# Kernel tuning notes

Measured on AMD Instinct MI355X. Metric: run time of the kernel, lower is better.

## Reference

```python
import jax, jax.numpy as jnp
import numpy as np

N = 100000
E = 3200000
OC = 16


def _lin_params(key, out_c, in_c, bias=True):
    k1, k2 = jax.random.split(key)
    s = 1.0 / np.sqrt(in_c)
    w = jax.random.uniform(k1, (out_c, in_c), jnp.float32, -s, s)
    b = jax.random.uniform(k2, (out_c,), jnp.float32, -s, s) if bias else None
    return w, b


def setup_inputs() -> dict:
    key = jax.random.key(0)
    ks = jax.random.split(key, 16)
    o = jax.random.normal(ks[0], (N, 2), jnp.float32)
    m = jax.random.normal(ks[1], (N, 2), jnp.float32)
    c = jax.random.uniform(ks[2], (N, 2), jnp.float32)
    ei_o = jax.random.randint(ks[3], (2, E), 0, N, jnp.int32)
    ei_m = jax.random.randint(ks[4], (2, E), 0, N, jnp.int32)
    ei_c = jax.random.randint(ks[5], (2, E), 0, N, jnp.int32)
    w1r, b1 = _lin_params(ks[6], 8, 2)
    w1s, _ = _lin_params(ks[7], 8, 2, bias=False)
    w2r, b2 = _lin_params(ks[8], OC, 8)
    w2s, _ = _lin_params(ks[9], OC, 8, bias=False)
    w3r, b3 = _lin_params(ks[10], OC, 2)
    w3s, _ = _lin_params(ks[11], OC, 2, bias=False)
    w4r, b4 = _lin_params(ks[12], 2, OC * 3)
    w4s, _ = _lin_params(ks[13], 2, OC * 3, bias=False)
    return dict(o=o, m=m, c=c, edge_index_o=ei_o, edge_index_m=ei_m, edge_index_c=ei_c,
                w1r=w1r, w1s=w1s, b1=b1, w2r=w2r, w2s=w2s, b2=b2,
                w3r=w3r, w3s=w3s, b3=b3, w4r=w4r, w4s=w4s, b4=b4)


def graph_conv(x, edge_index, w_rel, w_root, b):
    # PyG GraphConv, aggr='add': out_i = W_rel * sum_{j->i} x_j + b + W_root * x_i
    src, dst = edge_index[0], edge_index[1]
    agg = jax.ops.segment_sum(x[src], dst, num_segments=x.shape[0])
    return agg @ w_rel.T + b + x @ w_root.T


def forward_prior(x, ei, w1r, w1s, b1, w2r, w2s, b2):
    # dropout is identity in eval mode
    x = jax.nn.elu(graph_conv(x, ei, w1r, w1s, b1))
    return graph_conv(x, ei, w2r, w2s, b2)


def reference(o, m, c, edge_index_o, edge_index_m, edge_index_c,
              w1r, w1s, b1, w2r, w2s, b2, w3r, w3s, b3, w4r, w4s, b4):
    o_out = forward_prior(o, edge_index_o, w1r, w1s, b1, w2r, w2s, b2)
    o_feat = jnp.max(o_out, axis=0, keepdims=True)  # global_max_pool, single graph
    m_out = forward_prior(m, edge_index_m, w1r, w1s, b1, w2r, w2s, b2)
    m_feat = jnp.max(m_out, axis=0, keepdims=True)
    prior = jnp.concatenate([o_feat, m_feat], axis=1)  # [1, 2*OC]
    x = jax.nn.elu(graph_conv(c, edge_index_c, w3r, w3s, b3))  # [N, OC]
    x = jnp.concatenate([x, jnp.broadcast_to(prior, (c.shape[0], prior.shape[1]))], axis=1)
    x = graph_conv(x, edge_index_c, w4r, w4s, b4)
    return jax.nn.sigmoid(x) + c
```

## Files before the change

kernel.cpp:

```cpp
#include <hip/hip_runtime.h>
#include <float.h>
#include <math.h>


#define BBITS   8
#define BINSZ   256
#define MAXP    512
#define SRCBITS 17
#define SRCMASK ((1 << SRCBITS) - 1)
#define CAP     9216
#define EPT     8
#define EPT2    9

__device__ __forceinline__ float eluf(float x) {
  return x > 0.0f ? x : (expf(x) - 1.0f);
}

__device__ __forceinline__ void atomicMaxF(float* addr, float val) {
  int* ia = (int*)addr;
  int old = *ia;
  while (__int_as_float(old) < val) {
    int assumed = old;
    old = atomicCAS(ia, assumed, __float_as_int(val));
    if (old == assumed) break;
  }
}


__device__ __forceinline__ void place_body(const int* __restrict__ ei, int e, int P,
                                           int* __restrict__ binCnt, int* __restrict__ buf,
                                           int blk) {
  __shared__ int h[MAXP];
  __shared__ int base[MAXP];
  int t = threadIdx.x;
  for (int i = t; i < P; i += 1024) h[i] = 0;
  __syncthreads();
  const int* src = ei;
  const int* dst = ei + e;
  int lo = blk * (1024 * EPT);
  int v[EPT], bb[EPT], r[EPT];
#pragma unroll
  for (int k = 0; k < EPT; k++) {
    int idx = lo + k * 1024 + t;
    bool ok = idx < e;
    int d = ok ? dst[idx] : 0;
    int s = ok ? src[idx] : 0;
    bb[k] = ok ? (d >> BBITS) : -1;
    v[k] = ((d & (BINSZ - 1)) << SRCBITS) | s;
    r[k] = (bb[k] >= 0) ? atomicAdd(&h[bb[k]], 1) : 0;
  }
  __syncthreads();
  for (int i = t; i < P; i += 1024)
    base[i] = h[i] ? atomicAdd(&binCnt[i], h[i]) : 0;
  __syncthreads();
#pragma unroll
  for (int k = 0; k < EPT; k++) {
    if (bb[k] >= 0) {
      int idx = base[bb[k]] + r[k];
      if (idx < CAP) buf[(size_t)bb[k] * CAP + idx] = v[k];
    }
  }
}

__device__ __forceinline__ void sort_body(const int* __restrict__ binCnt,
                                          int* __restrict__ buf,
                                          int* __restrict__ rowBeg, int* __restrict__ rowEnd,
                                          int n, int p) {
  __shared__ int cnt[BINSZ];
  __shared__ int sc[BINSZ];
  int t = threadIdx.x;
  int nEd = min(binCnt[p], CAP);
  int* pk = buf + (size_t)p * CAP;
  if (t < BINSZ) cnt[t] = 0;
  __syncthreads();
  int v[EPT2], r[EPT2];
#pragma unroll
  for (int k = 0; k < EPT2; k++) {
    int i = k * 1024 + t;
    bool ok = i < nEd;
    v[k] = ok ? pk[i] : 0;
    r[k] = ok ? atomicAdd(&cnt[v[k] >> SRCBITS], 1) : -1;
  }
  __syncthreads();
  if (t < BINSZ) sc[t] = cnt[t];
  __syncthreads();
  for (int d = 1; d < BINSZ; d <<= 1) {
    int x = 0;
    if (t < BINSZ && t >= d) x = sc[t - d];
    __syncthreads();
    if (t < BINSZ) sc[t] += x;
    __syncthreads();
  }
  if (t < BINSZ) {
    int node = p * BINSZ + t;
    if (node < n) {
      int beg = p * CAP + sc[t] - cnt[t];
      rowBeg[node] = beg;
      rowEnd[node] = beg + cnt[t];
    }
  }
  __syncthreads();
#pragma unroll
  for (int k = 0; k < EPT2; k++) {
    if (r[k] >= 0) {
      int loc = v[k] >> SRCBITS;
      pk[sc[loc] - cnt[loc] + r[k]] = v[k] & SRCMASK;
    }
  }
}

__device__ __forceinline__ void agg1om_body(const int* __restrict__ rowBeg,
                                            const int* __restrict__ rowEnd,
                                            const int* __restrict__ src,
                                            const float* __restrict__ x,
                                            const float* __restrict__ wr,
                                            const float* __restrict__ b,
                                            const float* __restrict__ wo,
                                            float* __restrict__ xh8, int n, int tid) {
  int i = tid >> 3, j = tid & 7;
  if (i >= n) return;
  int r0 = rowBeg[i], r1 = rowEnd[i];
  float ax = 0.f, ay = 0.f;
  for (int e2 = r0 + j; e2 < r1; e2 += 8) {
    int s = src[e2];
    float2 v = ((const float2*)x)[s];
    ax += v.x;
    ay += v.y;
  }
  ax += __shfl_xor(ax, 1); ax += __shfl_xor(ax, 2); ax += __shfl_xor(ax, 4);
  ay += __shfl_xor(ay, 1); ay += __shfl_xor(ay, 2); ay += __shfl_xor(ay, 4);
  float2 xv = ((const float2*)x)[i];
  float v = eluf(wr[2 * j] * ax + wr[2 * j + 1] * ay + b[j] + wo[2 * j] * xv.x + wo[2 * j + 1] * xv.y);
  xh8[(size_t)i * 8 + j] = v;
}

__device__ __forceinline__ void agg2pool_body(const int* __restrict__ rowBeg,
                                              const int* __restrict__ rowEnd,
                                              const int* __restrict__ src,
                                              const float* __restrict__ x8,
                                              const float* __restrict__ wr,
                                              const float* __restrict__ b,
                                              const float* __restrict__ wo,
                                              float* __restrict__ bmax, int n,
                                              int tid, int aggblk) {
  __shared__ float wmax[16][16];
  int i = tid >> 3, j = tid & 7;
  float a[8] = {0, 0, 0, 0, 0, 0, 0, 0};
  bool valid = (i < n);
  if (valid) {
    int r0 = rowBeg[i], r1 = rowEnd[i];
    for (int e2 = r0 + j; e2 < r1; e2 += 8) {
      int s = src[e2];
      const float4* xp = (const float4*)(x8 + (size_t)s * 8);
      float4 v0 = xp[0], v1 = xp[1];
      a[0] += v0.x; a[1] += v0.y; a[2] += v0.z; a[3] += v0.w;
      a[4] += v1.x; a[5] += v1.y; a[6] += v1.z; a[7] += v1.w;
    }
  }
#pragma unroll
  for (int k = 0; k < 8; k++) {
    a[k] += __shfl_xor(a[k], 1);
    a[k] += __shfl_xor(a[k], 2);
    a[k] += __shfl_xor(a[k], 4);
  }
  float o0, o1;
  if (valid) {
    const float4* xp = (const float4*)(x8 + (size_t)i * 8);
    float4 x0 = xp[0], x1 = xp[1];
    float xx[8] = {x0.x, x0.y, x0.z, x0.w, x1.x, x1.y, x1.z, x1.w};
    int k0 = 2 * j, k1 = 2 * j + 1;
    o0 = b[k0];
    o1 = b[k1];
#pragma unroll
    for (int l = 0; l < 8; l++) {
      o0 += wr[8 * k0 + l] * a[l] + wo[8 * k0 + l] * xx[l];
      o1 += wr[8 * k1 + l] * a[l] + wo[8 * k1 + l] * xx[l];
    }
  } else {
    o0 = o1 = -FLT_MAX;
  }
#pragma unroll
  for (int d = 8; d < 64; d <<= 1) {
    o0 = fmaxf(o0, __shfl_xor(o0, d));
    o1 = fmaxf(o1, __shfl_xor(o1, d));
  }
  int wid = threadIdx.x >> 6, lane = threadIdx.x & 63;
  if (lane < 8) {
    wmax[wid][2 * lane] = o0;
    wmax[wid][2 * lane + 1] = o1;
  }
  __syncthreads();
  if (threadIdx.x < 16) {
    float v = -FLT_MAX;
#pragma unroll
    for (int w = 0; w < 16; w++) v = fmaxf(v, wmax[w][threadIdx.x]);
    bmax[(size_t)aggblk * 16 + threadIdx.x] = v;
  }
}


__global__ __launch_bounds__(1024) void place_k(const int* __restrict__ ei, int e, int P,
                                                int* __restrict__ binCnt, int* __restrict__ buf) {
  place_body(ei, e, P, binCnt, buf, blockIdx.x);
}

__global__ __launch_bounds__(1024) void sort_k(const int* __restrict__ binCnt,
                                               int* __restrict__ buf,
                                               int* __restrict__ rowBeg, int* __restrict__ rowEnd,
                                               int n) {
  sort_body(binCnt, buf, rowBeg, rowEnd, n, blockIdx.x);
}

__global__ __launch_bounds__(1024) void place_agg1_k(const int* __restrict__ eiX, int e, int P,
                                                     int* __restrict__ binCntX, int* __restrict__ bufX,
                                                     int EBP,
                                                     const int* __restrict__ rowBegY,
                                                     const int* __restrict__ rowEndY,
                                                     const int* __restrict__ srcY,
                                                     const float* __restrict__ xY,
                                                     const float* __restrict__ wr,
                                                     const float* __restrict__ b,
                                                     const float* __restrict__ wo,
                                                     float* __restrict__ xh8Y, int n) {
  if ((int)blockIdx.x < EBP) {
    place_body(eiX, e, P, binCntX, bufX, blockIdx.x);
    return;
  }
  int tid = (blockIdx.x - EBP) * 1024 + threadIdx.x;
  agg1om_body(rowBegY, rowEndY, srcY, xY, wr, b, wo, xh8Y, n, tid);
}

__global__ __launch_bounds__(1024) void sort_agg2_k(const int* __restrict__ binCntX,
                                                    int* __restrict__ bufX,
                                                    int* __restrict__ rowBegX,
                                                    int* __restrict__ rowEndX,
                                                    int n, int P,
                                                    const int* __restrict__ rowBegY,
                                                    const int* __restrict__ rowEndY,
                                                    const int* __restrict__ srcY,
                                                    const float* __restrict__ x8Y,
                                                    const float* __restrict__ wr,
                                                    const float* __restrict__ b,
                                                    const float* __restrict__ wo,
                                                    float* __restrict__ bmaxY) {
  if ((int)blockIdx.x < P) {
    sort_body(binCntX, bufX, rowBegX, rowEndX, n, blockIdx.x);
    return;
  }
  int aggblk = blockIdx.x - P;
  int tid = aggblk * 1024 + threadIdx.x;
  agg2pool_body(rowBegY, rowEndY, srcY, x8Y, wr, b, wo, bmaxY, n, tid, aggblk);
}

__global__ __launch_bounds__(1024) void agg1c_reduce_k(const float* __restrict__ bmax,
                                                       float* __restrict__ feats, int nb,
                                                       const int* __restrict__ rowBeg,
                                                       const int* __restrict__ rowEnd,
                                                       const int* __restrict__ src,
                                                       const float* __restrict__ cin,
                                                       const float* __restrict__ wr,
                                                       const float* __restrict__ b,
                                                       const float* __restrict__ wo,
                                                       const float* __restrict__ w4r,
                                                       const float* __restrict__ w4s,
                                                       float* __restrict__ yrel,
                                                       float* __restrict__ yroot, int n) {
  if (blockIdx.x == 0) {
    __shared__ float red[512];
    int t = threadIdx.x;
    if (t < 512) {
      int ch = t & 31, row = t >> 5;
      int g = ch >> 4, k = ch & 15;
      float v = -FLT_MAX;
      for (int blk = row; blk < nb; blk += 16)
        v = fmaxf(v, bmax[((size_t)g * nb + blk) * 16 + k]);
      red[t] = v;
    }
    __syncthreads();
    if (t < 32) {
      float m = red[t];
#pragma unroll
      for (int r = 1; r < 16; r++) m = fmaxf(m, red[t + 32 * r]);
      feats[t] = m;
    }
    return;
  }
  int tid = (blockIdx.x - 1) * 1024 + threadIdx.x;
  int i = tid >> 3, j = tid & 7;
  if (i >= n) return;
  int r0 = rowBeg[i], r1 = rowEnd[i];
  float ax = 0.f, ay = 0.f;
  for (int e2 = r0 + j; e2 < r1; e2 += 8) {
    int s = src[e2];
    float2 v = ((const float2*)cin)[s];
    ax += v.x;
    ay += v.y;
  }
  ax += __shfl_xor(ax, 1); ax += __shfl_xor(ax, 2); ax += __shfl_xor(ax, 4);
  ay += __shfl_xor(ay, 1); ay += __shfl_xor(ay, 2); ay += __shfl_xor(ay, 4);
  float2 xv = ((const float2*)cin)[i];
  float yr0 = 0.f, yr1 = 0.f, ys0 = 0.f, ys1 = 0.f;
#pragma unroll
  for (int kk = 0; kk < 2; kk++) {
    int k = 2 * j + kk;
    float v = eluf(wr[2 * k] * ax + wr[2 * k + 1] * ay + b[k] + wo[2 * k] * xv.x + wo[2 * k + 1] * xv.y);
    yr0 += w4r[k] * v;
    yr1 += w4r[48 + k] * v;
    ys0 += w4s[k] * v;
    ys1 += w4s[48 + k] * v;
  }
  yr0 += __shfl_xor(yr0, 1); yr0 += __shfl_xor(yr0, 2); yr0 += __shfl_xor(yr0, 4);
  yr1 += __shfl_xor(yr1, 1); yr1 += __shfl_xor(yr1, 2); yr1 += __shfl_xor(yr1, 4);
  ys0 += __shfl_xor(ys0, 1); ys0 += __shfl_xor(ys0, 2); ys0 += __shfl_xor(ys0, 4);
  ys1 += __shfl_xor(ys1, 1); ys1 += __shfl_xor(ys1, 2); ys1 += __shfl_xor(ys1, 4);
  if (j == 0) ((float2*)yrel)[i] = make_float2(yr0, yr1);
  if (j == 1) ((float2*)yroot)[i] = make_float2(ys0, ys1);
}

__global__ __launch_bounds__(1024) void aggfinal_k(const int* __restrict__ rowBeg,
                                                   const int* __restrict__ rowEnd,
                                                   const int* __restrict__ src,
                                                   const float* __restrict__ yrel,
                                                   const float* __restrict__ yroot,
                                                   const float* __restrict__ cin,
                                                   const float* __restrict__ feats,
                                                   const float* __restrict__ w4r,
                                                   const float* __restrict__ b4,
                                                   const float* __restrict__ w4s,
                                                   float* __restrict__ out, int n) {
  int tid = blockIdx.x * 1024 + threadIdx.x;
  int i = tid >> 3, j = tid & 7;
  if (i >= n) return;
  int r0 = rowBeg[i], r1 = rowEnd[i];
  float ay0 = 0.f, ay1 = 0.f;
  for (int e2 = r0 + j; e2 < r1; e2 += 8) {
    int s = src[e2];
    float2 v = ((const float2*)yrel)[s];
    ay0 += v.x;
    ay1 += v.y;
  }
  ay0 += __shfl_xor(ay0, 1); ay0 += __shfl_xor(ay0, 2); ay0 += __shfl_xor(ay0, 4);
  ay1 += __shfl_xor(ay1, 1); ay1 += __shfl_xor(ay1, 2); ay1 += __shfl_xor(ay1, 4);
  if (j != 0) return;
  float pr0 = 0.f, pr1 = 0.f, ps0 = 0.f, ps1 = 0.f;
#pragma unroll
  for (int k = 0; k < 32; k++) {
    float pv = feats[k];
    pr0 += w4r[16 + k] * pv;
    pr1 += w4r[64 + k] * pv;
    ps0 += w4s[16 + k] * pv;
    ps1 += w4s[64 + k] * pv;
  }
  float d = (float)(r1 - r0);
  float2 yrt = ((const float2*)yroot)[i];
  float acc0 = b4[0] + ps0 + d * pr0 + ay0 + yrt.x;
  float acc1 = b4[1] + ps1 + d * pr1 + ay1 + yrt.y;
  float2 cv = ((const float2*)cin)[i];
  float o0 = 1.0f / (1.0f + expf(-acc0)) + cv.x;
  float o1 = 1.0f / (1.0f + expf(-acc1)) + cv.y;
  ((float2*)out)[i] = make_float2(o0, o1);
}


__global__ void init_feats_k(float* feats) {
  int t = threadIdx.x;
  if (t < 32) feats[t] = -FLT_MAX;
}

__global__ void scatter2_k(const float* __restrict__ x, const int* __restrict__ ei,
                           float* __restrict__ agg, float* __restrict__ deg, int e) {
  int idx = blockIdx.x * blockDim.x + threadIdx.x;
  if (idx >= e) return;
  int s = ei[idx];
  int d = ei[e + idx];
  float2 v = ((const float2*)x)[s];
  atomicAdd(&agg[2 * d + 0], v.x);
  atomicAdd(&agg[2 * d + 1], v.y);
  if (deg) atomicAdd(&deg[d], 1.0f);
}

__global__ void scatter8_k(const float* __restrict__ x, const int* __restrict__ ei,
                           float* __restrict__ agg, int e) {
  int idx = blockIdx.x * blockDim.x + threadIdx.x;
  if (idx >= e) return;
  int s = ei[idx];
  int d = ei[e + idx];
  const float4* xp = (const float4*)(x + (size_t)s * 8);
  float4 v0 = xp[0], v1 = xp[1];
  float* ap = agg + (size_t)d * 8;
  atomicAdd(ap + 0, v0.x); atomicAdd(ap + 1, v0.y);
  atomicAdd(ap + 2, v0.z); atomicAdd(ap + 3, v0.w);
  atomicAdd(ap + 4, v1.x); atomicAdd(ap + 5, v1.y);
  atomicAdd(ap + 6, v1.z); atomicAdd(ap + 7, v1.w);
}

__global__ void scatter16_k(const float* __restrict__ x, const int* __restrict__ ei,
                            float* __restrict__ agg, int e) {
  int idx = blockIdx.x * blockDim.x + threadIdx.x;
  if (idx >= e) return;
  int s = ei[idx];
  int d = ei[e + idx];
  const float4* xp = (const float4*)(x + (size_t)s * 16);
  float4 v0 = xp[0], v1 = xp[1], v2 = xp[2], v3 = xp[3];
  float* ap = agg + (size_t)d * 16;
  atomicAdd(ap + 0,  v0.x); atomicAdd(ap + 1,  v0.y);
  atomicAdd(ap + 2,  v0.z); atomicAdd(ap + 3,  v0.w);
  atomicAdd(ap + 4,  v1.x); atomicAdd(ap + 5,  v1.y);
  atomicAdd(ap + 6,  v1.z); atomicAdd(ap + 7,  v1.w);
  atomicAdd(ap + 8,  v2.x); atomicAdd(ap + 9,  v2.y);
  atomicAdd(ap + 10, v2.z); atomicAdd(ap + 11, v2.w);
  atomicAdd(ap + 12, v3.x); atomicAdd(ap + 13, v3.y);
  atomicAdd(ap + 14, v3.z); atomicAdd(ap + 15, v3.w);
}

__global__ void node_2to8_elu_k(const float* __restrict__ agg, const float* __restrict__ xin,
                                const float* __restrict__ wr, const float* __restrict__ b,
                                const float* __restrict__ wo, float* __restrict__ xout, int n) {
  int i = blockIdx.x * blockDim.x + threadIdx.x;
  if (i >= n) return;
  float2 a = ((const float2*)agg)[i];
  float2 x = ((const float2*)xin)[i];
  float out[8];
#pragma unroll
  for (int k = 0; k < 8; k++)
    out[k] = eluf(wr[2 * k] * a.x + wr[2 * k + 1] * a.y + b[k] + wo[2 * k] * x.x + wo[2 * k + 1] * x.y);
  float4* op = (float4*)(xout + (size_t)i * 8);
  op[0] = make_float4(out[0], out[1], out[2], out[3]);
  op[1] = make_float4(out[4], out[5], out[6], out[7]);
}

__global__ void node_2to16_elu_k(const float* __restrict__ agg, const float* __restrict__ xin,
                                 const float* __restrict__ wr, const float* __restrict__ b,
                                 const float* __restrict__ wo, float* __restrict__ xout, int n) {
  int i = blockIdx.x * blockDim.x + threadIdx.x;
  if (i >= n) return;
  float2 a = ((const float2*)agg)[i];
  float2 x = ((const float2*)xin)[i];
  float out[16];
#pragma unroll
  for (int k = 0; k < 16; k++)
    out[k] = eluf(wr[2 * k] * a.x + wr[2 * k + 1] * a.y + b[k] + wo[2 * k] * x.x + wo[2 * k + 1] * x.y);
  float4* op = (float4*)(xout + (size_t)i * 16);
  op[0] = make_float4(out[0],  out[1],  out[2],  out[3]);
  op[1] = make_float4(out[4],  out[5],  out[6],  out[7]);
  op[2] = make_float4(out[8],  out[9],  out[10], out[11]);
  op[3] = make_float4(out[12], out[13], out[14], out[15]);
}

__global__ void conv2_pool_atomic_k(const float* __restrict__ agg, const float* __restrict__ x8,
                                    const float* __restrict__ wr, const float* __restrict__ b,
                                    const float* __restrict__ wo, float* __restrict__ feat, int n) {
  int i = blockIdx.x * blockDim.x + threadIdx.x;
  float out[16];
  if (i < n) {
    const float4* ap = (const float4*)(agg + (size_t)i * 8);
    const float4* xp = (const float4*)(x8 + (size_t)i * 8);
    float4 a0 = ap[0], a1 = ap[1];
    float4 x0 = xp[0], x1 = xp[1];
    float a[8] = {a0.x, a0.y, a0.z, a0.w, a1.x, a1.y, a1.z, a1.w};
    float x[8] = {x0.x, x0.y, x0.z, x0.w, x1.x, x1.y, x1.z, x1.w};
#pragma unroll
    for (int k = 0; k < 16; k++) {
      float v = b[k];
#pragma unroll
      for (int j = 0; j < 8; j++) v += wr[8 * k + j] * a[j] + wo[8 * k + j] * x[j];
      out[k] = v;
    }
  } else {
#pragma unroll
    for (int k = 0; k < 16; k++) out[k] = -FLT_MAX;
  }
#pragma unroll
  for (int k = 0; k < 16; k++) {
    float v = out[k];
    for (int off = 32; off >= 1; off >>= 1) v = fmaxf(v, __shfl_xor(v, off));
    if ((threadIdx.x & 63) == 0) atomicMaxF(&feat[k], v);
  }
}

__global__ void final_atomic_k(const float* __restrict__ agg16, const float* __restrict__ x16,
                               const float* __restrict__ deg, const float* __restrict__ cin,
                               const float* __restrict__ feats, const float* __restrict__ w4r,
                               const float* __restrict__ b4, const float* __restrict__ w4s,
                               float* __restrict__ out, int n) {
  int i = blockIdx.x * blockDim.x + threadIdx.x;
  if (i >= n) return;
  float pr0 = 0.f, pr1 = 0.f, ps0 = 0.f, ps1 = 0.f;
#pragma unroll
  for (int k = 0; k < 32; k++) {
    float pv = feats[k];
    pr0 += w4r[16 + k] * pv;
    pr1 += w4r[48 + 16 + k] * pv;
    ps0 += w4s[16 + k] * pv;
    ps1 += w4s[48 + 16 + k] * pv;
  }
  float d = deg[i];
  float acc0 = b4[0] + ps0 + d * pr0;
  float acc1 = b4[1] + ps1 + d * pr1;
  const float* ag = agg16 + (size_t)i * 16;
  const float* xv = x16 + (size_t)i * 16;
#pragma unroll
  for (int k = 0; k < 16; k++) {
    float a = ag[k], x = xv[k];
    acc0 += w4r[k] * a + w4s[k] * x;
    acc1 += w4r[48 + k] * a + w4s[48 + k] * x;
  }
  float2 cv = ((const float2*)cin)[i];
  float o0 = 1.0f / (1.0f + expf(-acc0)) + cv.x;
  float o1 = 1.0f / (1.0f + expf(-acc1)) + cv.y;
  ((float2*)out)[i] = make_float2(o0, o1);
}


extern "C" void kernel_launch(void* const* d_in, const int* in_sizes, int n_in,
                              void* d_out, int out_size, void* d_ws, size_t ws_size,
                              hipStream_t stream) {
  const float* o   = (const float*)d_in[0];
  const float* m   = (const float*)d_in[1];
  const float* c   = (const float*)d_in[2];
  const int* ei_o  = (const int*)d_in[3];
  const int* ei_m  = (const int*)d_in[4];
  const int* ei_c  = (const int*)d_in[5];
  const float* w1r = (const float*)d_in[6];
  const float* w1s = (const float*)d_in[7];
  const float* b1  = (const float*)d_in[8];
  const float* w2r = (const float*)d_in[9];
  const float* w2s = (const float*)d_in[10];
  const float* b2  = (const float*)d_in[11];
  const float* w3r = (const float*)d_in[12];
  const float* w3s = (const float*)d_in[13];
  const float* b3  = (const float*)d_in[14];
  const float* w4r = (const float*)d_in[15];
  const float* w4s = (const float*)d_in[16];
  const float* b4  = (const float*)d_in[17];

  const int n = in_sizes[0] / 2;
  const int e = in_sizes[3] / 2;
  const int P = (n + BINSZ - 1) >> BBITS;

  const int EBP = (e + 1024 * EPT - 1) / (1024 * EPT);
  const int G1  = (8 * n + 1023) / 1024;

  size_t off = 0;
  int* bufA = (int*)d_ws;                           off += (size_t)P * CAP * 4;
  int* bufB = (int*)((char*)d_ws + off);            off += (size_t)P * CAP * 4;
  int* rowBegA = (int*)((char*)d_ws + off);         off += (size_t)n * 4;
  int* rowEndA = (int*)((char*)d_ws + off);         off += (size_t)n * 4;
  int* rowBegB = (int*)((char*)d_ws + off);         off += (size_t)n * 4;
  int* rowEndB = (int*)((char*)d_ws + off);         off += (size_t)n * 4;
  float* xh8o = (float*)((char*)d_ws + off);        off += (size_t)n * 8 * 4;
  float* xh8m = (float*)((char*)d_ws + off);        off += (size_t)n * 8 * 4;
  float* bmax = (float*)((char*)d_ws + off);        off += (size_t)2 * G1 * 16 * 4;
  int* binCnt3 = (int*)((char*)d_ws + off);         off += (size_t)3 * MAXP * 4;
  float* feats = (float*)((char*)d_ws + off);       off += 32 * 4;

  float* yrel  = xh8o;
  float* yroot = xh8o + (size_t)2 * n;

  bool csr_ok = (off <= ws_size) && (P <= MAXP) && (n <= (1 << SRCBITS));

  if (!csr_ok) {
    const int BS = 256;
    const int nbn = (n + BS - 1) / BS;
    float* agg_f   = (float*)d_ws;
    float* xh_f    = agg_f + (size_t)n * 16;
    float* deg_f   = xh_f + (size_t)n * 16;
    float* feats_f = deg_f + n;
    const int nb_e = (e + BS - 1) / BS;
    init_feats_k<<<1, 64, 0, stream>>>(feats_f);
    hipMemsetAsync(agg_f, 0, (size_t)n * 2 * sizeof(float), stream);
    scatter2_k<<<nb_e, BS, 0, stream>>>(o, ei_o, agg_f, nullptr, e);
    node_2to8_elu_k<<<nbn, BS, 0, stream>>>(agg_f, o, w1r, b1, w1s, xh_f, n);
    hipMemsetAsync(agg_f, 0, (size_t)n * 8 * sizeof(float), stream);
    scatter8_k<<<nb_e, BS, 0, stream>>>(xh_f, ei_o, agg_f, e);
    conv2_pool_atomic_k<<<nbn, BS, 0, stream>>>(agg_f, xh_f, w2r, b2, w2s, feats_f, n);
    hipMemsetAsync(agg_f, 0, (size_t)n * 2 * sizeof(float), stream);
    scatter2_k<<<nb_e, BS, 0, stream>>>(m, ei_m, agg_f, nullptr, e);
    node_2to8_elu_k<<<nbn, BS, 0, stream>>>(agg_f, m, w1r, b1, w1s, xh_f, n);
    hipMemsetAsync(agg_f, 0, (size_t)n * 8 * sizeof(float), stream);
    scatter8_k<<<nb_e, BS, 0, stream>>>(xh_f, ei_m, agg_f, e);
    conv2_pool_atomic_k<<<nbn, BS, 0, stream>>>(agg_f, xh_f, w2r, b2, w2s, feats_f + 16, n);
    hipMemsetAsync(agg_f, 0, (size_t)n * 2 * sizeof(float), stream);
    hipMemsetAsync(deg_f, 0, (size_t)n * sizeof(float), stream);
    scatter2_k<<<nb_e, BS, 0, stream>>>(c, ei_c, agg_f, deg_f, e);
    node_2to16_elu_k<<<nbn, BS, 0, stream>>>(agg_f, c, w3r, b3, w3s, xh_f, n);
    hipMemsetAsync(agg_f, 0, (size_t)n * 16 * sizeof(float), stream);
    scatter16_k<<<nb_e, BS, 0, stream>>>(xh_f, ei_c, agg_f, e);
    final_atomic_k<<<nbn, BS, 0, stream>>>(agg_f, xh_f, deg_f, c, feats_f, w4r, b4, w4s,
                                           (float*)d_out, n);
    return;
  }

  int* bcO = binCnt3;
  int* bcM = binCnt3 + MAXP;
  int* bcC = binCnt3 + 2 * MAXP;

  hipMemsetAsync(binCnt3, 0, (size_t)3 * MAXP * sizeof(int), stream);

  place_k<<<EBP, 1024, 0, stream>>>(ei_o, e, P, bcO, bufA);
  sort_k<<<P, 1024, 0, stream>>>(bcO, bufA, rowBegA, rowEndA, n);

  place_agg1_k<<<EBP + G1, 1024, 0, stream>>>(ei_m, e, P, bcM, bufB, EBP,
                                              rowBegA, rowEndA, bufA, o,
                                              w1r, b1, w1s, xh8o, n);
  sort_agg2_k<<<P + G1, 1024, 0, stream>>>(bcM, bufB, rowBegB, rowEndB, n, P,
                                           rowBegA, rowEndA, bufA, xh8o,
                                           w2r, b2, w2s, bmax);

  place_agg1_k<<<EBP + G1, 1024, 0, stream>>>(ei_c, e, P, bcC, bufA, EBP,
                                              rowBegB, rowEndB, bufB, m,
                                              w1r, b1, w1s, xh8m, n);
  sort_agg2_k<<<P + G1, 1024, 0, stream>>>(bcC, bufA, rowBegA, rowEndA, n, P,
                                           rowBegB, rowEndB, bufB, xh8m,
                                           w2r, b2, w2s, bmax + (size_t)G1 * 16);

  agg1c_reduce_k<<<1 + G1, 1024, 0, stream>>>(bmax, feats, G1,
                                              rowBegA, rowEndA, bufA, c,
                                              w3r, b3, w3s, w4r, w4s,
                                              yrel, yroot, n);
  aggfinal_k<<<G1, 1024, 0, stream>>>(rowBegA, rowEndA, bufA, yrel, yroot, c,
                                      feats, w4r, b4, w4s, (float*)d_out, n);
}
```

Before: 279.1 us.

## Add third CSR buffer to deepen cross-graph pipeline of sort/place/aggregate kernels

Allocates a third bucket buffer so the CSR build for graph c no longer has to wait for graph o's buffer to be freed. The independent stages of the three graphs (place, sort, agg1, agg2, agg1c) are then packed into fewer, wider fused launches: 7 kernels instead of 8, with more concurrent blocks each. The global feature reduction is split into its own small kernel. This costs more workspace, and a fallback two-buffer schedule is kept for when the workspace is too small.

```diff
diff --git a/kernel.cpp b/kernel.cpp
--- a/kernel.cpp
+++ b/kernel.cpp
@@ -198,94 +198,17 @@
   }
 }
 
-
-__global__ __launch_bounds__(1024) void place_k(const int* __restrict__ ei, int e, int P,
-                                                int* __restrict__ binCnt, int* __restrict__ buf) {
-  place_body(ei, e, P, binCnt, buf, blockIdx.x);
-}
-
-__global__ __launch_bounds__(1024) void sort_k(const int* __restrict__ binCnt,
-                                               int* __restrict__ buf,
-                                               int* __restrict__ rowBeg, int* __restrict__ rowEnd,
-                                               int n) {
-  sort_body(binCnt, buf, rowBeg, rowEnd, n, blockIdx.x);
-}
-
-__global__ __launch_bounds__(1024) void place_agg1_k(const int* __restrict__ eiX, int e, int P,
-                                                     int* __restrict__ binCntX, int* __restrict__ bufX,
-                                                     int EBP,
-                                                     const int* __restrict__ rowBegY,
-                                                     const int* __restrict__ rowEndY,
-                                                     const int* __restrict__ srcY,
-                                                     const float* __restrict__ xY,
-                                                     const float* __restrict__ wr,
-                                                     const float* __restrict__ b,
-                                                     const float* __restrict__ wo,
-                                                     float* __restrict__ xh8Y, int n) {
-  if ((int)blockIdx.x < EBP) {
-    place_body(eiX, e, P, binCntX, bufX, blockIdx.x);
-    return;
-  }
-  int tid = (blockIdx.x - EBP) * 1024 + threadIdx.x;
-  agg1om_body(rowBegY, rowEndY, srcY, xY, wr, b, wo, xh8Y, n, tid);
-}
-
-__global__ __launch_bounds__(1024) void sort_agg2_k(const int* __restrict__ binCntX,
-                                                    int* __restrict__ bufX,
-                                                    int* __restrict__ rowBegX,
-                                                    int* __restrict__ rowEndX,
-                                                    int n, int P,
-                                                    const int* __restrict__ rowBegY,
-                                                    const int* __restrict__ rowEndY,
-                                                    const int* __restrict__ srcY,
-                                                    const float* __restrict__ x8Y,
-                                                    const float* __restrict__ wr,
-                                                    const float* __restrict__ b,
-                                                    const float* __restrict__ wo,
-                                                    float* __restrict__ bmaxY) {
-  if ((int)blockIdx.x < P) {
-    sort_body(binCntX, bufX, rowBegX, rowEndX, n, blockIdx.x);
-    return;
-  }
-  int aggblk = blockIdx.x - P;
-  int tid = aggblk * 1024 + threadIdx.x;
-  agg2pool_body(rowBegY, rowEndY, srcY, x8Y, wr, b, wo, bmaxY, n, tid, aggblk);
-}
-
-__global__ __launch_bounds__(1024) void agg1c_reduce_k(const float* __restrict__ bmax,
-                                                       float* __restrict__ feats, int nb,
-                                                       const int* __restrict__ rowBeg,
-                                                       const int* __restrict__ rowEnd,
-                                                       const int* __restrict__ src,
-                                                       const float* __restrict__ cin,
-                                                       const float* __restrict__ wr,
-                                                       const float* __restrict__ b,
-                                                       const float* __restrict__ wo,
-                                                       const float* __restrict__ w4r,
-                                                       const float* __restrict__ w4s,
-                                                       float* __restrict__ yrel,
-                                                       float* __restrict__ yroot, int n) {
-  if (blockIdx.x == 0) {
-    __shared__ float red[512];
-    int t = threadIdx.x;
-    if (t < 512) {
-      int ch = t & 31, row = t >> 5;
-      int g = ch >> 4, k = ch & 15;
-      float v = -FLT_MAX;
-      for (int blk = row; blk < nb; blk += 16)
-        v = fmaxf(v, bmax[((size_t)g * nb + blk) * 16 + k]);
-      red[t] = v;
-    }
-    __syncthreads();
-    if (t < 32) {
-      float m = red[t];
-#pragma unroll
-      for (int r = 1; r < 16; r++) m = fmaxf(m, red[t + 32 * r]);
-      feats[t] = m;
-    }
-    return;
-  }
-  int tid = (blockIdx.x - 1) * 1024 + threadIdx.x;
+__device__ __forceinline__ void agg1c_body(const int* __restrict__ rowBeg,
+                                           const int* __restrict__ rowEnd,
+                                           const int* __restrict__ src,
+                                           const float* __restrict__ cin,
+                                           const float* __restrict__ wr,
+                                           const float* __restrict__ b,
+                                           const float* __restrict__ wo,
+                                           const float* __restrict__ w4r,
+                                           const float* __restrict__ w4s,
+                                           float* __restrict__ yrel,
+                                           float* __restrict__ yroot, int n, int tid) {
   int i = tid >> 3, j = tid & 7;
   if (i >= n) return;
   int r0 = rowBeg[i], r1 = rowEnd[i];
@@ -315,6 +238,103 @@
   ys1 += __shfl_xor(ys1, 1); ys1 += __shfl_xor(ys1, 2); ys1 += __shfl_xor(ys1, 4);
   if (j == 0) ((float2*)yrel)[i] = make_float2(yr0, yr1);
   if (j == 1) ((float2*)yroot)[i] = make_float2(ys0, ys1);
+}
+
+
+__global__ __launch_bounds__(1024) void place_k(const int* __restrict__ ei, int e, int P,
+                                                int* __restrict__ binCnt, int* __restrict__ buf) {
+  place_body(ei, e, P, binCnt, buf, blockIdx.x);
+}
+
+__global__ __launch_bounds__(1024) void k_sort_place(const int* __restrict__ bcX,
+                                                     int* __restrict__ bufX,
+                                                     int* __restrict__ rbX, int* __restrict__ reX,
+                                                     int n, int P,
+                                                     const int* __restrict__ eiY, int e,
+                                                     int* __restrict__ bcY, int* __restrict__ bufY) {
+  int b = blockIdx.x;
+  if (b < P) { sort_body(bcX, bufX, rbX, reX, n, b); return; }
+  place_body(eiY, e, P, bcY, bufY, b - P);
+}
+
+__global__ __launch_bounds__(1024) void k_sort_place_agg1(
+    int nS, int nPl,
+    const int* __restrict__ bcY, int* __restrict__ bufY,
+    int* __restrict__ rbY, int* __restrict__ reY, int n, int P,
+    const int* __restrict__ eiZ, int e,
+    int* __restrict__ bcZ, int* __restrict__ bufZ,
+    const int* __restrict__ rbX, const int* __restrict__ reX,
+    const int* __restrict__ srcX, const float* __restrict__ xX,
+    const float* __restrict__ w1r, const float* __restrict__ b1,
+    const float* __restrict__ w1s, float* __restrict__ xh8X) {
+  int b = blockIdx.x;
+  if (b < nS) { sort_body(bcY, bufY, rbY, reY, n, b); return; }
+  b -= nS;
+  if (b < nPl) { place_body(eiZ, e, P, bcZ, bufZ, b); return; }
+  b -= nPl;
+  agg1om_body(rbX, reX, srcX, xX, w1r, b1, w1s, xh8X, n, b * 1024 + threadIdx.x);
+}
+
+__global__ __launch_bounds__(1024) void k_sort_agg1_agg2(
+    int nS, int nA1,
+    const int* __restrict__ bcZ, int* __restrict__ bufZ,
+    int* __restrict__ rbZ, int* __restrict__ reZ, int n, int P,
+    const int* __restrict__ rbY, const int* __restrict__ reY,
+    const int* __restrict__ srcY, const float* __restrict__ xY,
+    const float* __restrict__ w1r, const float* __restrict__ b1,
+    const float* __restrict__ w1s, float* __restrict__ xh8Y,
+    const int* __restrict__ rbX, const int* __restrict__ reX,
+    const int* __restrict__ srcX, const float* __restrict__ x8X,
+    const float* __restrict__ w2r, const float* __restrict__ b2,
+    const float* __restrict__ w2s, float* __restrict__ bmaxX) {
+  int b = blockIdx.x;
+  if (b < nS) { sort_body(bcZ, bufZ, rbZ, reZ, n, b); return; }
+  b -= nS;
+  if (b < nA1) { agg1om_body(rbY, reY, srcY, xY, w1r, b1, w1s, xh8Y, n, b * 1024 + threadIdx.x); return; }
+  b -= nA1;
+  agg2pool_body(rbX, reX, srcX, x8X, w2r, b2, w2s, bmaxX, n, b * 1024 + threadIdx.x, b);
+}
+
+__global__ __launch_bounds__(1024) void k_agg1c_agg2(
+    int nA1c,
+    const int* __restrict__ rbC, const int* __restrict__ reC,
+    const int* __restrict__ srcC, const float* __restrict__ cin,
+    const float* __restrict__ w3r, const float* __restrict__ b3,
+    const float* __restrict__ w3s,
+    const float* __restrict__ w4r, const float* __restrict__ w4s,
+    float* __restrict__ yrel, float* __restrict__ yroot, int n,
+    const int* __restrict__ rbY, const int* __restrict__ reY,
+    const int* __restrict__ srcY, const float* __restrict__ x8Y,
+    const float* __restrict__ w2r, const float* __restrict__ b2,
+    const float* __restrict__ w2s, float* __restrict__ bmaxY) {
+  int b = blockIdx.x;
+  if (b < nA1c) {
+    agg1c_body(rbC, reC, srcC, cin, w3r, b3, w3s, w4r, w4s, yrel, yroot, n,
+               b * 1024 + threadIdx.x);
+    return;
+  }
+  b -= nA1c;
+  agg2pool_body(rbY, reY, srcY, x8Y, w2r, b2, w2s, bmaxY, n,
+                b * 1024 + threadIdx.x, b);
+}
+
+__global__ void reduce_feats_k(const float* __restrict__ bmax, float* __restrict__ feats,
+                               int nb) {
+  __shared__ float red[512];
+  int t = threadIdx.x;
+  int ch = t & 31, row = t >> 5;
+  int g = ch >> 4, k = ch & 15;
+  float v = -FLT_MAX;
+  for (int blk = row; blk < nb; blk += 16)
+    v = fmaxf(v, bmax[((size_t)g * nb + blk) * 16 + k]);
+  red[t] = v;
+  __syncthreads();
+  if (t < 32) {
+    float m = red[t];
+#pragma unroll
+    for (int r = 1; r < 16; r++) m = fmaxf(m, red[t + 32 * r]);
+    feats[t] = m;
+  }
 }
 
 __global__ __launch_bounds__(1024) void aggfinal_k(const int* __restrict__ rowBeg,
@@ -541,25 +561,116 @@
   const int EBP = (e + 1024 * EPT - 1) / (1024 * EPT);
   const int G1  = (8 * n + 1023) / 1024;
 
-  size_t off = 0;
-  int* bufA = (int*)d_ws;                           off += (size_t)P * CAP * 4;
-  int* bufB = (int*)((char*)d_ws + off);            off += (size_t)P * CAP * 4;
-  int* rowBegA = (int*)((char*)d_ws + off);         off += (size_t)n * 4;
-  int* rowEndA = (int*)((char*)d_ws + off);         off += (size_t)n * 4;
-  int* rowBegB = (int*)((char*)d_ws + off);         off += (size_t)n * 4;
-  int* rowEndB = (int*)((char*)d_ws + off);         off += (size_t)n * 4;
-  float* xh8o = (float*)((char*)d_ws + off);        off += (size_t)n * 8 * 4;
-  float* xh8m = (float*)((char*)d_ws + off);        off += (size_t)n * 8 * 4;
-  float* bmax = (float*)((char*)d_ws + off);        off += (size_t)2 * G1 * 16 * 4;
-  int* binCnt3 = (int*)((char*)d_ws + off);         off += (size_t)3 * MAXP * 4;
-  float* feats = (float*)((char*)d_ws + off);       off += 32 * 4;
+  const size_t slab = (size_t)P * CAP * 4;
+
+  size_t off3 = 0;
+  int* bufA = (int*)d_ws;                            off3 += slab;
+  int* bufB = (int*)((char*)d_ws + off3);            off3 += slab;
+  int* bufC = (int*)((char*)d_ws + off3);            off3 += slab;
+  int* rbA = (int*)((char*)d_ws + off3);             off3 += (size_t)n * 4;
+  int* reA = (int*)((char*)d_ws + off3);             off3 += (size_t)n * 4;
+  int* rbB = (int*)((char*)d_ws + off3);             off3 += (size_t)n * 4;
+  int* reB = (int*)((char*)d_ws + off3);             off3 += (size_t)n * 4;
+  int* rbC = (int*)((char*)d_ws + off3);             off3 += (size_t)n * 4;
+  int* reC = (int*)((char*)d_ws + off3);             off3 += (size_t)n * 4;
+  float* xh8o = (float*)((char*)d_ws + off3);        off3 += (size_t)n * 8 * 4;
+  float* xh8m = (float*)((char*)d_ws + off3);        off3 += (size_t)n * 8 * 4;
+  float* bmax = (float*)((char*)d_ws + off3);        off3 += (size_t)2 * G1 * 16 * 4;
+  int* binCnt3 = (int*)((char*)d_ws + off3);         off3 += (size_t)3 * MAXP * 4;
+  float* feats = (float*)((char*)d_ws + off3);       off3 += 32 * 4;
 
   float* yrel  = xh8o;
   float* yroot = xh8o + (size_t)2 * n;
 
-  bool csr_ok = (off <= ws_size) && (P <= MAXP) && (n <= (1 << SRCBITS));
-
-  if (!csr_ok) {
+  bool ok_base = (P <= MAXP) && (n <= (1 << SRCBITS));
+  bool deep_ok = ok_base && (off3 <= ws_size);
+
+  if (deep_ok) {
+    int* bcO = binCnt3;
+    int* bcM = binCnt3 + MAXP;
+    int* bcC = binCnt3 + 2 * MAXP;
+    hipMemsetAsync(binCnt3, 0, (size_t)3 * MAXP * sizeof(int), stream);
+
+    place_k<<<EBP, 1024, 0, stream>>>(ei_o, e, P, bcO, bufA);
+    k_sort_place<<<P + EBP, 1024, 0, stream>>>(bcO, bufA, rbA, reA, n, P,
+                                               ei_m, e, bcM, bufB);
+    k_sort_place_agg1<<<P + EBP + G1, 1024, 0, stream>>>(
+        P, EBP,
+        bcM, bufB, rbB, reB, n, P,
+        ei_c, e, bcC, bufC,
+        rbA, reA, bufA, o, w1r, b1, w1s, xh8o);
+    k_sort_agg1_agg2<<<P + G1 + G1, 1024, 0, stream>>>(
+        P, G1,
+        bcC, bufC, rbC, reC, n, P,
+        rbB, reB, bufB, m, w1r, b1, w1s, xh8m,
+        rbA, reA, bufA, xh8o, w2r, b2, w2s, bmax);
+    k_agg1c_agg2<<<G1 + G1, 1024, 0, stream>>>(
+        G1,
+        rbC, reC, bufC, c, w3r, b3, w3s, w4r, w4s, yrel, yroot, n,
+        rbB, reB, bufB, xh8m, w2r, b2, w2s, bmax + (size_t)G1 * 16);
+    reduce_feats_k<<<1, 512, 0, stream>>>(bmax, feats, G1);
+    aggfinal_k<<<G1, 1024, 0, stream>>>(rbC, reC, bufC, yrel, yroot, c,
+                                        feats, w4r, b4, w4s, (float*)d_out, n);
+    return;
+  }
+
+  size_t off2 = 0;
+  int* bufA2 = (int*)d_ws;                           off2 += slab;
+  int* bufB2 = (int*)((char*)d_ws + off2);           off2 += slab;
+  int* rbA2 = (int*)((char*)d_ws + off2);            off2 += (size_t)n * 4;
+  int* reA2 = (int*)((char*)d_ws + off2);            off2 += (size_t)n * 4;
+  int* rbB2 = (int*)((char*)d_ws + off2);            off2 += (size_t)n * 4;
+  int* reB2 = (int*)((char*)d_ws + off2);            off2 += (size_t)n * 4;
+  float* xh8o2 = (float*)((char*)d_ws + off2);       off2 += (size_t)n * 8 * 4;
+  float* xh8m2 = (float*)((char*)d_ws + off2);       off2 += (size_t)n * 8 * 4;
+  float* bmax2 = (float*)((char*)d_ws + off2);       off2 += (size_t)2 * G1 * 16 * 4;
+  int* binCnt32 = (int*)((char*)d_ws + off2);        off2 += (size_t)3 * MAXP * 4;
+  float* feats2 = (float*)((char*)d_ws + off2);      off2 += 32 * 4;
+  float* yrel2  = xh8o2;
+  float* yroot2 = xh8o2 + (size_t)2 * n;
+
+  bool two_ok = ok_base && (off2 <= ws_size);
+
+  if (two_ok) {
+    int* bcO = binCnt32;
+    int* bcM = binCnt32 + MAXP;
+    int* bcC = binCnt32 + 2 * MAXP;
+    hipMemsetAsync(binCnt32, 0, (size_t)3 * MAXP * sizeof(int), stream);
+
+    place_k<<<EBP, 1024, 0, stream>>>(ei_o, e, P, bcO, bufA2);
+    k_sort_place<<<P + EBP, 1024, 0, stream>>>(bcO, bufA2, rbA2, reA2, n, P,
+                                               ei_m, e, bcM, bufB2);
+    k_sort_place_agg1<<<P + G1, 1024, 0, stream>>>(
+        P, 0,
+        bcM, bufB2, rbB2, reB2, n, P,
+        ei_c, e, bcC, bufA2,
+        rbA2, reA2, bufA2, o, w1r, b1, w1s, xh8o2);
+    k_sort_agg1_agg2<<<G1, 1024, 0, stream>>>(
+        0, 0,
+        bcC, bufA2, rbA2, reA2, n, P,
+        rbB2, reB2, bufB2, m, w1r, b1, w1s, xh8m2,
+        rbA2, reA2, bufA2, xh8o2, w2r, b2, w2s, bmax2);
+    k_sort_place_agg1<<<EBP + G1, 1024, 0, stream>>>(
+        0, EBP,
+        bcM, bufB2, rbB2, reB2, n, P,
+        ei_c, e, bcC, bufA2,
+        rbB2, reB2, bufB2, m, w1r, b1, w1s, xh8m2);
+    k_sort_agg1_agg2<<<P + G1, 1024, 0, stream>>>(
+        P, 0,
+        bcC, bufA2, rbA2, reA2, n, P,
+        rbB2, reB2, bufB2, m, w1r, b1, w1s, xh8m2,
+        rbB2, reB2, bufB2, xh8m2, w2r, b2, w2s, bmax2 + (size_t)G1 * 16);
+    reduce_feats_k<<<1, 512, 0, stream>>>(bmax2, feats2, G1);
+    k_agg1c_agg2<<<G1, 1024, 0, stream>>>(
+        G1,
+        rbA2, reA2, bufA2, c, w3r, b3, w3s, w4r, w4s, yrel2, yroot2, n,
+        rbB2, reB2, bufB2, xh8m2, w2r, b2, w2s, bmax2);
+    aggfinal_k<<<G1, 1024, 0, stream>>>(rbA2, reA2, bufA2, yrel2, yroot2, c,
+                                        feats2, w4r, b4, w4s, (float*)d_out, n);
+    return;
+  }
+
+  {
     const int BS = 256;
     const int nbn = (n + BS - 1) / BS;
     float* agg_f   = (float*)d_ws;
@@ -588,36 +699,5 @@
     scatter16_k<<<nb_e, BS, 0, stream>>>(xh_f, ei_c, agg_f, e);
     final_atomic_k<<<nbn, BS, 0, stream>>>(agg_f, xh_f, deg_f, c, feats_f, w4r, b4, w4s,
                                            (float*)d_out, n);
-    return;
-  }
-
-  int* bcO = binCnt3;
-  int* bcM = binCnt3 + MAXP;
-  int* bcC = binCnt3 + 2 * MAXP;
-
-  hipMemsetAsync(binCnt3, 0, (size_t)3 * MAXP * sizeof(int), stream);
-
-  place_k<<<EBP, 1024, 0, stream>>>(ei_o, e, P, bcO, bufA);
-  sort_k<<<P, 1024, 0, stream>>>(bcO, bufA, rowBegA, rowEndA, n);
-
-  place_agg1_k<<<EBP + G1, 1024, 0, stream>>>(ei_m, e, P, bcM, bufB, EBP,
-                                              rowBegA, rowEndA, bufA, o,
-                                              w1r, b1, w1s, xh8o, n);
-  sort_agg2_k<<<P + G1, 1024, 0, stream>>>(bcM, bufB, rowBegB, rowEndB, n, P,
-                                           rowBegA, rowEndA, bufA, xh8o,
-                                           w2r, b2, w2s, bmax);
-
-  place_agg1_k<<<EBP + G1, 1024, 0, stream>>>(ei_c, e, P, bcC, bufA, EBP,
-                                              rowBegB, rowEndB, bufB, m,
-                                              w1r, b1, w1s, xh8m, n);
-  sort_agg2_k<<<P + G1, 1024, 0, stream>>>(bcC, bufA, rowBegA, rowEndA, n, P,
-                                           rowBegB, rowEndB, bufB, xh8m,
-                                           w2r, b2, w2s, bmax + (size_t)G1 * 16);
-
-  agg1c_reduce_k<<<1 + G1, 1024, 0, stream>>>(bmax, feats, G1,
-                                              rowBegA, rowEndA, bufA, c,
-                                              w3r, b3, w3s, w4r, w4s,
-                                              yrel, yroot, n);
-  aggfinal_k<<<G1, 1024, 0, stream>>>(rowBegA, rowEndA, bufA, yrel, yroot, c,
-                                      feats, w4r, b4, w4s, (float*)d_out, n);
-}
+  }
+}
```

After: 285.5 us. +2.3%, slower.
